# Performance work log

Measured on AMD Instinct MI355X. Metric: run time of the kernel, lower is better.

## Reference

```python
import jax, jax.numpy as jnp
import numpy as np

N_NODES, N_EDGES = 100000, 800000
F_NODE, F_EDGE, N_CLASSES = 128, 16, 10


def _lin(key, fan_in, fan_out, bias=True):
    k1, k2 = jax.random.split(key)
    W = jax.random.normal(k1, (fan_in, fan_out), jnp.float32) * 0.05
    if bias:
        b = jax.random.normal(k2, (fan_out,), jnp.float32) * 0.05
        return W, b
    return (W,)


def setup_inputs() -> dict:
    key = jax.random.key(0)
    ks = jax.random.split(key, 24)
    inp = {
        "x": jax.random.normal(ks[0], (N_NODES, F_NODE), jnp.float32),
        "edge_index": jax.random.randint(ks[1], (2, N_EDGES), 0, N_NODES, jnp.int64 if jax.config.jax_enable_x64 else jnp.int32),
        "edge_attr": jax.random.normal(ks[2], (N_EDGES, F_EDGE), jnp.float32),
    }
    dims = [(F_NODE, 128), (128, 128), (128, 256)]  # (in_channels, out_channels) per layer
    i = 3
    for li, (din, dout) in enumerate(dims, start=1):
        inp[f"Wq{li}"], inp[f"bq{li}"] = _lin(ks[i], din, dout); i += 1
        inp[f"Wk{li}"], inp[f"bk{li}"] = _lin(ks[i], din, dout); i += 1
        inp[f"Wv{li}"], inp[f"bv{li}"] = _lin(ks[i], din, dout); i += 1
        (inp[f"We{li}"],) = _lin(ks[i], F_EDGE, dout, bias=False); i += 1  # PyG lin_edge: bias=False
        inp[f"Ws{li}"], inp[f"bs{li}"] = _lin(ks[i], din, dout); i += 1  # root/skip weight
    inp["Wc"], inp["bc"] = _lin(ks[i], 256, N_CLASSES)
    return inp


def transformer_conv(x, src, dst, edge_attr, Wq, bq, Wk, bk, Wv, bv, We, Ws, bs):
    """PyG TransformerConv, heads=1, concat=True, root_weight=True."""
    N = x.shape[0]
    C = Wq.shape[1]
    q = x @ Wq + bq                      # [N, C]
    k = x @ Wk + bk                      # [N, C]
    v = x @ Wv + bv                      # [N, C]
    e = edge_attr @ We                   # [E, C] edge-conditioned term
    # per-edge attention logits: <q_i, k_j + e_ij> / sqrt(C)
    alpha = jnp.sum(q[dst] * (k[src] + e), axis=-1) / jnp.sqrt(jnp.float32(C))  # [E]
    # segment softmax over edges sharing a destination node
    m = jax.ops.segment_max(alpha, dst, num_segments=N)
    p = jnp.exp(alpha - m[dst])
    s = jax.ops.segment_sum(p, dst, num_segments=N)
    a = p / (s[dst] + 1e-16)
    # scatter-aggregate weighted messages (value_j + edge term)
    out = jax.ops.segment_sum(a[:, None] * (v[src] + e), dst, num_segments=N)  # [N, C]
    return out + x @ Ws + bs             # root/skip connection


def reference(x, edge_index, edge_attr,
              Wq1, bq1, Wk1, bk1, Wv1, bv1, We1, Ws1, bs1,
              Wq2, bq2, Wk2, bk2, Wv2, bv2, We2, Ws2, bs2,
              Wq3, bq3, Wk3, bk3, Wv3, bv3, We3, Ws3, bs3,
              Wc, bc):
    src, dst = edge_index[0], edge_index[1]
    h = transformer_conv(x, src, dst, edge_attr, Wq1, bq1, Wk1, bk1, Wv1, bv1, We1, Ws1, bs1)
    h = jax.nn.relu(h)  # dropout is identity in eval mode
    h = transformer_conv(h, src, dst, edge_attr, Wq2, bq2, Wk2, bk2, Wv2, bv2, We2, Ws2, bs2)
    h = jax.nn.relu(h)
    h = transformer_conv(h, src, dst, edge_attr, Wq3, bq3, Wk3, bk3, Wv3, bv3, We3, Ws3, bs3)
    return h @ Wc + bc                   # [N, num_classes]
```

## Files before the change

### kernel.cpp

```cpp
#include <hip/hip_runtime.h>
#include <math.h>


typedef unsigned int uint;
typedef unsigned short ushort;
typedef __bf16 bf16x8 __attribute__((ext_vector_type(8)));
typedef float f32x4 __attribute__((ext_vector_type(4)));

__device__ __forceinline__ ushort f2bf(float f) {
    uint u = __float_as_uint(f);
    u += 0x7fffu + ((u >> 16) & 1u);
    return (ushort)(u >> 16);
}
__device__ __forceinline__ float bf2f(ushort h) {
    return __uint_as_float(((uint)h) << 16);
}
__device__ __forceinline__ void unpack8(uint4 t, float* o) {
    o[0] = bf2f((ushort)(t.x & 0xffffu)); o[1] = bf2f((ushort)(t.x >> 16));
    o[2] = bf2f((ushort)(t.y & 0xffffu)); o[3] = bf2f((ushort)(t.y >> 16));
    o[4] = bf2f((ushort)(t.z & 0xffffu)); o[5] = bf2f((ushort)(t.z >> 16));
    o[6] = bf2f((ushort)(t.w & 0xffffu)); o[7] = bf2f((ushort)(t.w >> 16));
}

__global__ void k_zero(uint* p, int n) {
    int i = blockIdx.x * 256 + threadIdx.x;
    if (i < n) p[i] = 0u;
}

__global__ void k_hist(const int* __restrict__ dst, uint* __restrict__ counts, int E, int N) {
    int e = blockIdx.x * 256 + threadIdx.x;
    if (e < E) {
        int d = dst[e];
        d = (d < 0) ? 0 : (d >= N ? N - 1 : d);
        atomicAdd(&counts[d], 1u);
    }
}

__global__ void k_scan1(const uint* __restrict__ counts, uint* __restrict__ bsum, int n) {
    __shared__ uint sm[256];
    int tid = threadIdx.x;
    int base = blockIdx.x * 1024 + tid * 4;
    uint s = 0;
#pragma unroll
    for (int j = 0; j < 4; ++j)
        if (base + j < n) s += counts[base + j];
    sm[tid] = s;
    __syncthreads();
    for (int d = 128; d > 0; d >>= 1) {
        if (tid < d) sm[tid] += sm[tid + d];
        __syncthreads();
    }
    if (tid == 0) bsum[blockIdx.x] = sm[0];
}

__global__ void k_scan2(uint* bsum, int nb) {
    if (threadIdx.x == 0 && blockIdx.x == 0) {
        uint run = 0;
        for (int i = 0; i < nb; ++i) { uint v = bsum[i]; bsum[i] = run; run += v; }
    }
}

__global__ void k_scan3(const uint* __restrict__ counts, const uint* __restrict__ bsum,
                        uint* __restrict__ row_ptr, int n, int E) {
    __shared__ uint sm[256];
    int tid = threadIdx.x;
    int base = blockIdx.x * 1024 + tid * 4;
    uint local[4];
    uint s = 0;
#pragma unroll
    for (int j = 0; j < 4; ++j) {
        local[j] = (base + j < n) ? counts[base + j] : 0u;
        s += local[j];
    }
    sm[tid] = s;
    __syncthreads();
    for (int d = 1; d < 256; d <<= 1) {
        uint v = (tid >= d) ? sm[tid - d] : 0u;
        __syncthreads();
        sm[tid] += v;
        __syncthreads();
    }
    uint run = sm[tid] - s + bsum[blockIdx.x];
#pragma unroll
    for (int j = 0; j < 4; ++j)
        if (base + j < n) { row_ptr[base + j] = run; run += local[j]; }
    if (blockIdx.x == 0 && tid == 0) row_ptr[n] = (uint)E;
}

__global__ void k_fill(const int* __restrict__ ei, const uint* __restrict__ row_ptr,
                       uint* __restrict__ cursor, int2* __restrict__ srcid, int E, int N) {
    int e = blockIdx.x * 256 + threadIdx.x;
    if (e >= E) return;
    int s = ei[e];
    int d = ei[E + e];
    s = (s < 0) ? 0 : (s >= N ? N - 1 : s);
    d = (d < 0) ? 0 : (d >= N ? N - 1 : d);
    uint idx = row_ptr[d] + atomicAdd(&cursor[d], 1u);
    srcid[idx] = make_int2(s, e);
}

__global__ void k_cvt(const float4* __restrict__ in, ushort4* __restrict__ outp, int n4) {
    int i = blockIdx.x * 256 + threadIdx.x;
    if (i >= n4) return;
    float4 v = in[i];
    ushort4 o;
    o.x = f2bf(v.x); o.y = f2bf(v.y); o.z = f2bf(v.z); o.w = f2bf(v.w);
    outp[i] = o;
}

__global__ void k_packg(const float* __restrict__ Wq, const float* __restrict__ bq,
                        const float* __restrict__ We, float* __restrict__ Wgf,
                        float* __restrict__ bgf, int C) {
    int id = blockIdx.x * 256 + threadIdx.x;
    if (id < 2048) {
        int k = id >> 4, f = id & 15;
        float s = 0.f;
        for (int c = 0; c < C; ++c) s = fmaf(Wq[k * C + c], We[f * C + c], s);
        Wgf[id] = s;
    } else if (id < 2064) {
        int f = id - 2048;
        float s = 0.f;
        for (int c = 0; c < C; ++c) s = fmaf(bq[c], We[f * C + c], s);
        bgf[f] = s;
    }
}

__global__ void k_packw(const float* __restrict__ Wq, const float* __restrict__ Wk,
                        const float* __restrict__ Wv, const float* __restrict__ Ws,
                        const float* __restrict__ Wgf, ushort* __restrict__ Bp, int C) {
    int nct = (4 * C + 16) >> 4;
    int total = 4 * nct * 512;
    int id = blockIdx.x * 256 + threadIdx.x;
    if (id >= total) return;
    int j = id & 7;
    int rest = id >> 3;
    int lane = rest & 63;
    rest >>= 6;
    int ct = rest % nct;
    int kt = rest / nct;
    int k = kt * 32 + ((lane >> 4) << 3) + j;
    int c = (ct << 4) + (lane & 15);
    float w;
    if (c < 4 * C) {
        int mat = c / C, cc = c % C;
        const float* W = (mat == 0) ? Wq : (mat == 1) ? Wk : (mat == 2) ? Wv : Ws;
        w = W[k * C + cc];
    } else {
        w = Wgf[k * 16 + (c - 4 * C)];
    }
    Bp[id] = f2bf(w);
}

__global__ void k_bias(const float* __restrict__ bq, const float* __restrict__ bk,
                       const float* __restrict__ bv, const float* __restrict__ bs,
                       const float* __restrict__ bgf, float* __restrict__ outp, int C) {
    int c = blockIdx.x * 256 + threadIdx.x;
    if (c >= 4 * C + 16) return;
    float v;
    if (c < 4 * C) {
        int mat = c / C, cc = c % C;
        const float* b = (mat == 0) ? bq : (mat == 1) ? bk : (mat == 2) ? bv : bs;
        v = b[cc];
    } else {
        v = bgf[c - 4 * C];
    }
    outp[c] = v;
}

__global__ __launch_bounds__(256) void k_gemm(const ushort* __restrict__ A,
                                              const ushort* __restrict__ Bp,
                                              const float* __restrict__ bias,
                                              ushort* __restrict__ H,
                                              ushort* __restrict__ S,
                                              ushort* __restrict__ g, int C) {
    int fourC = 4 * C, threeC = 3 * C;
    int P = fourC + 16;
    int nct = P >> 4;
    int lane = threadIdx.x & 63;
    int wave = threadIdx.x >> 6;
    int quad = lane >> 4;
    int r = lane & 15;
    int m0 = blockIdx.y << 4;
    int c0 = (blockIdx.x << 8) + (wave << 6);
    int ct0 = c0 >> 4;
    if (ct0 >= nct) return;
    int row = m0 + r;

    f32x4 acc[4];
#pragma unroll
    for (int i = 0; i < 4; ++i) acc[i] = (f32x4){0.f, 0.f, 0.f, 0.f};

#pragma unroll
    for (int kk = 0; kk < 4; ++kk) {
        bf16x8 a = *(const bf16x8*)(A + (size_t)row * 128 + kk * 32 + (quad << 3));
#pragma unroll
        for (int i = 0; i < 4; ++i) {
            if (ct0 + i < nct) {
                bf16x8 b = *(const bf16x8*)(Bp + ((size_t)((kk * nct + ct0 + i) << 6) + lane) * 8);
                acc[i] = __builtin_amdgcn_mfma_f32_16x16x32_bf16(a, b, acc[i], 0, 0, 0);
            }
        }
    }
#pragma unroll
    for (int i = 0; i < 4; ++i) {
        int cc = c0 + (i << 4) + r;
        if (cc >= P) continue;
        float bi = bias[cc];
#pragma unroll
        for (int reg = 0; reg < 4; ++reg) {
            int rr = m0 + (quad << 2) + reg;
            ushort val = f2bf(acc[i][reg] + bi);
            if (cc < threeC)      H[(size_t)rr * threeC + cc] = val;
            else if (cc < fourC)  S[(size_t)rr * C + (cc - threeC)] = val;
            else                  g[(size_t)rr * 16 + (cc - fourC)] = val;
        }
    }
}

template <int C, int GSIZE, bool RELU>
__global__ __launch_bounds__(256, 6) void k_edge(const ushort* __restrict__ H,
                                                 ushort* __restrict__ S,
                                                 const ushort* __restrict__ g,
                                                 const uint* __restrict__ row_ptr,
                                                 const int2* __restrict__ srcid,
                                                 const float* __restrict__ eattr,
                                                 const float* __restrict__ We,
                                                 int N) {
    constexpr int VR = C / GSIZE;
    constexpr int TH = 3 * C;
    constexpr int GPB = 256 / GSIZE;
    __shared__ float swex[GPB][17];
    const float scale = (C == 128) ? 0.08838834764831843f : 0.0625f;
    const float foldk = 16.0f / (float)GSIZE;

    int lane = threadIdx.x & (GSIZE - 1);
    int grp = threadIdx.x / GSIZE;
    int f = lane & 15;
    int node = blockIdx.x * GPB + grp;
    if (node >= N) return;

    float q[VR];
    {
        uint4 tt = *(const uint4*)(H + (size_t)node * TH + lane * VR);
        unpack8(tt, q);
    }
    float gl = bf2f(g[(size_t)node * 16 + f]);
    uint beg = row_ptr[node], end = row_ptr[node + 1];

    float l = 0.f, w = 0.f;
    float acc[VR];
#pragma unroll
    for (int j = 0; j < VR; ++j) acc[j] = 0.f;

    for (uint t = beg; t < end; t += 2) {
        bool has1 = (t + 1 < end);
        int2 se0 = srcid[t];
        int2 se1 = has1 ? srcid[t + 1] : se0;
        float at0 = eattr[(size_t)se0.y * 16 + f];
        float at1 = eattr[(size_t)se1.y * 16 + f];
        uint4 k0 = *(const uint4*)(H + (size_t)se0.x * TH + C + lane * VR);
        uint4 v0 = *(const uint4*)(H + (size_t)se0.x * TH + 2 * C + lane * VR);
        uint4 k1, v1;
        if (has1) {
            k1 = *(const uint4*)(H + (size_t)se1.x * TH + C + lane * VR);
            v1 = *(const uint4*)(H + (size_t)se1.x * TH + 2 * C + lane * VR);
        }
        float kf[VR];
        unpack8(k0, kf);
        float p0 = foldk * at0 * gl;
#pragma unroll
        for (int j = 0; j < VR; ++j) p0 = fmaf(q[j], kf[j], p0);
        float p1 = 0.f;
        if (has1) {
            unpack8(k1, kf);
            p1 = foldk * at1 * gl;
#pragma unroll
            for (int j = 0; j < VR; ++j) p1 = fmaf(q[j], kf[j], p1);
        }
        p0 += __shfl_xor(p0, 1); p1 += __shfl_xor(p1, 1);
        p0 += __shfl_xor(p0, 2); p1 += __shfl_xor(p1, 2);
        p0 += __shfl_xor(p0, 4); p1 += __shfl_xor(p1, 4);
        p0 += __shfl_xor(p0, 8); p1 += __shfl_xor(p1, 8);
        if (GSIZE == 32) { p0 += __shfl_xor(p0, 16); p1 += __shfl_xor(p1, 16); }
        float e0 = __expf(p0 * scale);
        float e1 = has1 ? __expf(p1 * scale) : 0.f;
        l += e0 + e1;
        w = fmaf(e0, at0, w);
        w = fmaf(e1, at1, w);
        float vf[VR];
        unpack8(v0, vf);
#pragma unroll
        for (int j = 0; j < VR; ++j) acc[j] = fmaf(e0, vf[j], acc[j]);
        if (has1) {
            unpack8(v1, vf);
#pragma unroll
            for (int j = 0; j < VR; ++j) acc[j] = fmaf(e1, vf[j], acc[j]);
        }
    }

    float inv = 1.f / (l + 1e-16f);
    if (lane < 16) swex[grp][lane] = w;
    float ew[VR];
#pragma unroll
    for (int j = 0; j < VR; ++j) ew[j] = 0.f;
#pragma unroll
    for (int f2 = 0; f2 < 16; ++f2) {
        float wf = swex[grp][f2];
        const float* wrow = We + f2 * C + lane * VR;
#pragma unroll
        for (int u = 0; u < VR / 4; ++u) {
            float4 cv = *(const float4*)(wrow + u * 4);
            ew[u * 4 + 0] = fmaf(wf, cv.x, ew[u * 4 + 0]);
            ew[u * 4 + 1] = fmaf(wf, cv.y, ew[u * 4 + 1]);
            ew[u * 4 + 2] = fmaf(wf, cv.z, ew[u * 4 + 2]);
            ew[u * 4 + 3] = fmaf(wf, cv.w, ew[u * 4 + 3]);
        }
    }
    ushort* srow = S + (size_t)node * C + lane * VR;
    uint4 skv = *(const uint4*)srow;
    float sk[8];
    unpack8(skv, sk);
    uint4 ov;
    uint* op = (uint*)&ov;
#pragma unroll
    for (int h = 0; h < 4; ++h) {
        float o0 = (acc[2 * h] + ew[2 * h]) * inv + sk[2 * h];
        float o1 = (acc[2 * h + 1] + ew[2 * h + 1]) * inv + sk[2 * h + 1];
        if (RELU) { o0 = fmaxf(o0, 0.f); o1 = fmaxf(o1, 0.f); }
        op[h] = (uint)f2bf(o0) | ((uint)f2bf(o1) << 16);
    }
    *(uint4*)srow = ov;
}

__global__ void k_cls(const ushort* __restrict__ h, const float* __restrict__ Wc,
                      const float* __restrict__ bc, float* __restrict__ outp, int N) {
    int t = blockIdx.x * 256 + threadIdx.x;
    int node = t >> 4;
    int c = t & 15;
    if (node >= N || c >= 10) return;
    const ushort* hr = h + (size_t)node * 256;
    float acc = 0.f;
#pragma unroll 4
    for (int k4 = 0; k4 < 64; ++k4) {
        uint2 u = *(const uint2*)(hr + k4 * 4);
        float h0 = bf2f((ushort)(u.x & 0xffffu));
        float h1 = bf2f((ushort)(u.x >> 16));
        float h2 = bf2f((ushort)(u.y & 0xffffu));
        float h3 = bf2f((ushort)(u.y >> 16));
        int kb = k4 * 4;
        acc = fmaf(h0, Wc[(kb + 0) * 10 + c], acc);
        acc = fmaf(h1, Wc[(kb + 1) * 10 + c], acc);
        acc = fmaf(h2, Wc[(kb + 2) * 10 + c], acc);
        acc = fmaf(h3, Wc[(kb + 3) * 10 + c], acc);
    }
    outp[node * 10 + c] = acc + bc[c];
}

extern "C" void kernel_launch(void* const* d_in, const int* in_sizes, int n_in,
                              void* d_out, int out_size, void* d_ws, size_t ws_size,
                              hipStream_t stream) {
    const float* x = (const float*)d_in[0];
    const int* ei = (const int*)d_in[1];
    const float* eattr = (const float*)d_in[2];
    const int N = in_sizes[0] / 128;
    const int E = in_sizes[1] / 2;

    const float* Wq[3], *bq[3], *Wk[3], *bk[3], *Wv[3], *bv[3], *We[3], *Ws[3], *bs[3];
    for (int li = 0; li < 3; ++li) {
        int base = 3 + li * 9;
        Wq[li] = (const float*)d_in[base + 0];
        bq[li] = (const float*)d_in[base + 1];
        Wk[li] = (const float*)d_in[base + 2];
        bk[li] = (const float*)d_in[base + 3];
        Wv[li] = (const float*)d_in[base + 4];
        bv[li] = (const float*)d_in[base + 5];
        We[li] = (const float*)d_in[base + 6];
        Ws[li] = (const float*)d_in[base + 7];
        bs[li] = (const float*)d_in[base + 8];
    }
    const float* Wc = (const float*)d_in[30];
    const float* bc = (const float*)d_in[31];

    size_t off = 0;
    char* base = (char*)d_ws;
    auto alloc = [&](size_t bytes) -> void* {
        void* p = base + off;
        off = (off + bytes + 255) & ~(size_t)255;
        return p;
    };
    ushort* SA = (ushort*)alloc((size_t)N * 256 * 2);
    ushort* SB = (ushort*)alloc((size_t)N * 128 * 2);
    ushort* H  = (ushort*)alloc((size_t)N * 768 * 2);
    ushort* gbuf = (ushort*)alloc((size_t)N * 16 * 2);
    ushort* Bp = (ushort*)alloc(140000 * 2);
    float* biasc = (float*)alloc(1040 * 4);
    float* Wgf = (float*)alloc(2048 * 4);
    float* bgf = (float*)alloc(16 * 4);
    uint* row_ptr = (uint*)alloc((size_t)(N + 1) * 4);
    uint* counts = (uint*)alloc((size_t)N * 4);
    uint* cursor = (uint*)alloc((size_t)N * 4);
    uint* bsum = (uint*)alloc(1024 * 4);
    int2* srcid = (int2*)alloc((size_t)E * 8);

    ushort* xb = SB;

    int nb = (N + 1023) / 1024;

    k_zero<<<(N + 255) / 256, 256, 0, stream>>>(counts, N);
    k_zero<<<(N + 255) / 256, 256, 0, stream>>>(cursor, N);
    k_hist<<<(E + 255) / 256, 256, 0, stream>>>(ei + E, counts, E, N);
    k_scan1<<<nb, 256, 0, stream>>>(counts, bsum, N);
    k_scan2<<<1, 64, 0, stream>>>(bsum, nb);
    k_scan3<<<nb, 256, 0, stream>>>(counts, bsum, row_ptr, N, E);
    k_fill<<<(E + 255) / 256, 256, 0, stream>>>(ei, row_ptr, cursor, srcid, E, N);

    int n4 = N * 128 / 4;
    k_cvt<<<(n4 + 255) / 256, 256, 0, stream>>>((const float4*)x, (ushort4*)xb, n4);

    for (int li = 0; li < 3; ++li) {
        int C = (li == 2) ? 256 : 128;
        int P = 4 * C + 16;
        int packTotal = 4 * (P >> 4) * 512;
        const ushort* A = (li == 0) ? xb : (li == 1) ? SA : SB;
        ushort* Sout = (li == 1) ? SB : SA;

        k_packg<<<9, 256, 0, stream>>>(Wq[li], bq[li], We[li], Wgf, bgf, C);
        k_packw<<<(packTotal + 255) / 256, 256, 0, stream>>>(Wq[li], Wk[li], Wv[li], Ws[li], Wgf, Bp, C);
        k_bias<<<(P + 255) / 256, 256, 0, stream>>>(bq[li], bk[li], bv[li], bs[li], bgf, biasc, C);
        k_gemm<<<dim3((P + 255) / 256, N / 16), 256, 0, stream>>>(A, Bp, biasc, H, Sout, gbuf, C);
        if (li == 2)
            k_edge<256, 32, false><<<(N * 32 + 255) / 256, 256, 0, stream>>>(H, Sout, gbuf, row_ptr, srcid, eattr, We[li], N);
        else
            k_edge<128, 16, true><<<(N * 16 + 255) / 256, 256, 0, stream>>>(H, Sout, gbuf, row_ptr, srcid, eattr, We[li], N);
    }

    k_cls<<<(N * 16 + 255) / 256, 256, 0, stream>>>(SA, Wc, bc, (float*)d_out, N);
}
```

Baseline: 1.021 ms.

## Fuse classifier into last edge kernel, permute edge attrs, enlarge GEMM tiles

Edge attributes are now permuted into CSR order as bf16 during the fill pass, so the edge kernel reads them contiguously and prefetches the next pair's source ids and attributes one iteration ahead. The GEMM processes 64 rows per block, reusing each B fragment across four row tiles, and handles a ragged N. Weight and bias packing merge into one kernel, the zeroing launches merge into one, and the final classifier is fused into the last edge kernel through a shuffle reduction. The aims are fewer launches, less scattered edge-attribute traffic and better GEMM operand reuse, at the cost of more registers in the GEMM and edge kernels and bf16 rounding of edge attributes.

Result: slower. 1.183 ms (+15.8%).

```diff
diff --git a/kernel.cpp b/kernel.cpp
--- a/kernel.cpp
+++ b/kernel.cpp
@@ -87,8 +87,9 @@
     if (blockIdx.x == 0 && tid == 0) row_ptr[n] = (uint)E;
 }
 
-__global__ void k_fill(const int* __restrict__ ei, const uint* __restrict__ row_ptr,
-                       uint* __restrict__ cursor, int2* __restrict__ srcid, int E, int N) {
+__global__ void k_fill(const int* __restrict__ ei, const float* __restrict__ eattr,
+                       const uint* __restrict__ row_ptr, uint* __restrict__ cursor,
+                       int* __restrict__ srci, ushort* __restrict__ eperm, int E, int N) {
     int e = blockIdx.x * 256 + threadIdx.x;
     if (e >= E) return;
     int s = ei[e];
@@ -96,7 +97,20 @@
     s = (s < 0) ? 0 : (s >= N ? N - 1 : s);
     d = (d < 0) ? 0 : (d >= N ? N - 1 : d);
     uint idx = row_ptr[d] + atomicAdd(&cursor[d], 1u);
-    srcid[idx] = make_int2(s, e);
+    srci[idx] = s;
+    const float4* sv = (const float4*)(eattr + (size_t)e * 16);
+    float4 a0 = sv[0], a1 = sv[1], a2 = sv[2], a3 = sv[3];
+    uint4 o0, o1;
+    o0.x = (uint)f2bf(a0.x) | ((uint)f2bf(a0.y) << 16);
+    o0.y = (uint)f2bf(a0.z) | ((uint)f2bf(a0.w) << 16);
+    o0.z = (uint)f2bf(a1.x) | ((uint)f2bf(a1.y) << 16);
+    o0.w = (uint)f2bf(a1.z) | ((uint)f2bf(a1.w) << 16);
+    o1.x = (uint)f2bf(a2.x) | ((uint)f2bf(a2.y) << 16);
+    o1.y = (uint)f2bf(a2.z) | ((uint)f2bf(a2.w) << 16);
+    o1.z = (uint)f2bf(a3.x) | ((uint)f2bf(a3.y) << 16);
+    o1.w = (uint)f2bf(a3.z) | ((uint)f2bf(a3.w) << 16);
+    *(uint4*)(eperm + (size_t)idx * 16) = o0;
+    *(uint4*)(eperm + (size_t)idx * 16 + 8) = o1;
 }
 
 __global__ void k_cvt(const float4* __restrict__ in, ushort4* __restrict__ outp, int n4) {
@@ -125,46 +139,46 @@
     }
 }
 
-__global__ void k_packw(const float* __restrict__ Wq, const float* __restrict__ Wk,
-                        const float* __restrict__ Wv, const float* __restrict__ Ws,
-                        const float* __restrict__ Wgf, ushort* __restrict__ Bp, int C) {
-    int nct = (4 * C + 16) >> 4;
+__global__ void k_packwb(const float* __restrict__ Wq, const float* __restrict__ bq,
+                         const float* __restrict__ Wk, const float* __restrict__ bk,
+                         const float* __restrict__ Wv, const float* __restrict__ bv,
+                         const float* __restrict__ Ws, const float* __restrict__ bs,
+                         const float* __restrict__ Wgf, const float* __restrict__ bgf,
+                         ushort* __restrict__ Bp, float* __restrict__ biasc, int C) {
+    int P = 4 * C + 16;
+    int nct = P >> 4;
     int total = 4 * nct * 512;
     int id = blockIdx.x * 256 + threadIdx.x;
-    if (id >= total) return;
-    int j = id & 7;
-    int rest = id >> 3;
-    int lane = rest & 63;
-    rest >>= 6;
-    int ct = rest % nct;
-    int kt = rest / nct;
-    int k = kt * 32 + ((lane >> 4) << 3) + j;
-    int c = (ct << 4) + (lane & 15);
-    float w;
-    if (c < 4 * C) {
-        int mat = c / C, cc = c % C;
-        const float* W = (mat == 0) ? Wq : (mat == 1) ? Wk : (mat == 2) ? Wv : Ws;
-        w = W[k * C + cc];
-    } else {
-        w = Wgf[k * 16 + (c - 4 * C)];
-    }
-    Bp[id] = f2bf(w);
-}
-
-__global__ void k_bias(const float* __restrict__ bq, const float* __restrict__ bk,
-                       const float* __restrict__ bv, const float* __restrict__ bs,
-                       const float* __restrict__ bgf, float* __restrict__ outp, int C) {
-    int c = blockIdx.x * 256 + threadIdx.x;
-    if (c >= 4 * C + 16) return;
-    float v;
-    if (c < 4 * C) {
-        int mat = c / C, cc = c % C;
-        const float* b = (mat == 0) ? bq : (mat == 1) ? bk : (mat == 2) ? bv : bs;
-        v = b[cc];
-    } else {
-        v = bgf[c - 4 * C];
-    }
-    outp[c] = v;
+    if (id < total) {
+        int j = id & 7;
+        int rest = id >> 3;
+        int lane = rest & 63;
+        rest >>= 6;
+        int ct = rest % nct;
+        int kt = rest / nct;
+        int k = kt * 32 + ((lane >> 4) << 3) + j;
+        int c = (ct << 4) + (lane & 15);
+        float w;
+        if (c < 4 * C) {
+            int mat = c / C, cc = c % C;
+            const float* W = (mat == 0) ? Wq : (mat == 1) ? Wk : (mat == 2) ? Wv : Ws;
+            w = W[k * C + cc];
+        } else {
+            w = Wgf[k * 16 + (c - 4 * C)];
+        }
+        Bp[id] = f2bf(w);
+    } else if (id < total + P) {
+        int c = id - total;
+        float v;
+        if (c < 4 * C) {
+            int mat = c / C, cc = c % C;
+            const float* b = (mat == 0) ? bq : (mat == 1) ? bk : (mat == 2) ? bv : bs;
+            v = b[cc];
+        } else {
+            v = bgf[c - 4 * C];
+        }
+        biasc[c] = v;
+    }
 }
 
 __global__ __launch_bounds__(256) void k_gemm(const ushort* __restrict__ A,
@@ -172,7 +186,7 @@
                                               const float* __restrict__ bias,
                                               ushort* __restrict__ H,
                                               ushort* __restrict__ S,
-                                              ushort* __restrict__ g, int C) {
+                                              ushort* __restrict__ g, int C, int N) {
     int fourC = 4 * C, threeC = 3 * C;
     int P = fourC + 16;
     int nct = P >> 4;
@@ -180,51 +194,66 @@
     int wave = threadIdx.x >> 6;
     int quad = lane >> 4;
     int r = lane & 15;
-    int m0 = blockIdx.y << 4;
-    int c0 = (blockIdx.x << 8) + (wave << 6);
-    int ct0 = c0 >> 4;
+    int m0 = blockIdx.y << 6;
+    int ct0 = (blockIdx.x << 4) + (wave << 2);
     if (ct0 >= nct) return;
-    int row = m0 + r;
-
-    f32x4 acc[4];
-#pragma unroll
-    for (int i = 0; i < 4; ++i) acc[i] = (f32x4){0.f, 0.f, 0.f, 0.f};
+
+    f32x4 acc[4][4];
+#pragma unroll
+    for (int rt = 0; rt < 4; ++rt)
+#pragma unroll
+        for (int i = 0; i < 4; ++i) acc[rt][i] = (f32x4){0.f, 0.f, 0.f, 0.f};
 
 #pragma unroll
     for (int kk = 0; kk < 4; ++kk) {
-        bf16x8 a = *(const bf16x8*)(A + (size_t)row * 128 + kk * 32 + (quad << 3));
+        bf16x8 a[4];
+#pragma unroll
+        for (int rt = 0; rt < 4; ++rt) {
+            int row = m0 + rt * 16 + r;
+            if (row >= N) row = N - 1;
+            a[rt] = *(const bf16x8*)(A + (size_t)row * 128 + kk * 32 + (quad << 3));
+        }
 #pragma unroll
         for (int i = 0; i < 4; ++i) {
             if (ct0 + i < nct) {
                 bf16x8 b = *(const bf16x8*)(Bp + ((size_t)((kk * nct + ct0 + i) << 6) + lane) * 8);
-                acc[i] = __builtin_amdgcn_mfma_f32_16x16x32_bf16(a, b, acc[i], 0, 0, 0);
+#pragma unroll
+                for (int rt = 0; rt < 4; ++rt)
+                    acc[rt][i] = __builtin_amdgcn_mfma_f32_16x16x32_bf16(a[rt], b, acc[rt][i], 0, 0, 0);
             }
         }
     }
 #pragma unroll
     for (int i = 0; i < 4; ++i) {
-        int cc = c0 + (i << 4) + r;
+        int cc = ((ct0 + i) << 4) + r;
         if (cc >= P) continue;
         float bi = bias[cc];
 #pragma unroll
-        for (int reg = 0; reg < 4; ++reg) {
-            int rr = m0 + (quad << 2) + reg;
-            ushort val = f2bf(acc[i][reg] + bi);
-            if (cc < threeC)      H[(size_t)rr * threeC + cc] = val;
-            else if (cc < fourC)  S[(size_t)rr * C + (cc - threeC)] = val;
-            else                  g[(size_t)rr * 16 + (cc - fourC)] = val;
-        }
-    }
-}
-
-template <int C, int GSIZE, bool RELU>
+        for (int rt = 0; rt < 4; ++rt) {
+#pragma unroll
+            for (int reg = 0; reg < 4; ++reg) {
+                int rr = m0 + rt * 16 + (quad << 2) + reg;
+                if (rr >= N) continue;
+                ushort val = f2bf(acc[rt][i][reg] + bi);
+                if (cc < threeC)      H[(size_t)rr * threeC + cc] = val;
+                else if (cc < fourC)  S[(size_t)rr * C + (cc - threeC)] = val;
+                else                  g[(size_t)rr * 16 + (cc - fourC)] = val;
+            }
+        }
+    }
+}
+
+template <int C, int GSIZE, bool RELU, bool FUSECLS>
 __global__ __launch_bounds__(256, 6) void k_edge(const ushort* __restrict__ H,
                                                  ushort* __restrict__ S,
                                                  const ushort* __restrict__ g,
                                                  const uint* __restrict__ row_ptr,
-                                                 const int2* __restrict__ srcid,
-                                                 const float* __restrict__ eattr,
+                                                 const int* __restrict__ srci,
+                                                 const ushort* __restrict__ eperm,
                                                  const float* __restrict__ We,
+                                                 const float* __restrict__ Wc,
+                                                 const float* __restrict__ bc,
+                                                 float* __restrict__ outp,
                                                  int N) {
     constexpr int VR = C / GSIZE;
     constexpr int TH = 3 * C;
@@ -252,49 +281,60 @@
 #pragma unroll
     for (int j = 0; j < VR; ++j) acc[j] = 0.f;
 
-    for (uint t = beg; t < end; t += 2) {
-        bool has1 = (t + 1 < end);
-        int2 se0 = srcid[t];
-        int2 se1 = has1 ? srcid[t + 1] : se0;
-        float at0 = eattr[(size_t)se0.y * 16 + f];
-        float at1 = eattr[(size_t)se1.y * 16 + f];
-        uint4 k0 = *(const uint4*)(H + (size_t)se0.x * TH + C + lane * VR);
-        uint4 v0 = *(const uint4*)(H + (size_t)se0.x * TH + 2 * C + lane * VR);
-        uint4 k1, v1;
-        if (has1) {
-            k1 = *(const uint4*)(H + (size_t)se1.x * TH + C + lane * VR);
-            v1 = *(const uint4*)(H + (size_t)se1.x * TH + 2 * C + lane * VR);
-        }
-        float kf[VR];
-        unpack8(k0, kf);
-        float p0 = foldk * at0 * gl;
-#pragma unroll
-        for (int j = 0; j < VR; ++j) p0 = fmaf(q[j], kf[j], p0);
-        float p1 = 0.f;
-        if (has1) {
-            unpack8(k1, kf);
-            p1 = foldk * at1 * gl;
-#pragma unroll
-            for (int j = 0; j < VR; ++j) p1 = fmaf(q[j], kf[j], p1);
-        }
-        p0 += __shfl_xor(p0, 1); p1 += __shfl_xor(p1, 1);
-        p0 += __shfl_xor(p0, 2); p1 += __shfl_xor(p1, 2);
-        p0 += __shfl_xor(p0, 4); p1 += __shfl_xor(p1, 4);
-        p0 += __shfl_xor(p0, 8); p1 += __shfl_xor(p1, 8);
-        if (GSIZE == 32) { p0 += __shfl_xor(p0, 16); p1 += __shfl_xor(p1, 16); }
-        float e0 = __expf(p0 * scale);
-        float e1 = has1 ? __expf(p1 * scale) : 0.f;
-        l += e0 + e1;
-        w = fmaf(e0, at0, w);
-        w = fmaf(e1, at1, w);
-        float vf[VR];
-        unpack8(v0, vf);
-#pragma unroll
-        for (int j = 0; j < VR; ++j) acc[j] = fmaf(e0, vf[j], acc[j]);
-        if (has1) {
-            unpack8(v1, vf);
-#pragma unroll
-            for (int j = 0; j < VR; ++j) acc[j] = fmaf(e1, vf[j], acc[j]);
+    if (beg < end) {
+        bool h1 = (beg + 1 < end);
+        int s0 = srci[beg];
+        int s1 = h1 ? srci[beg + 1] : s0;
+        float a0 = bf2f(eperm[(size_t)beg * 16 + f]);
+        float a1 = h1 ? bf2f(eperm[(size_t)(beg + 1) * 16 + f]) : 0.f;
+        for (uint t = beg; t < end; t += 2) {
+            uint4 k0 = *(const uint4*)(H + (size_t)s0 * TH + C + lane * VR);
+            uint4 v0 = *(const uint4*)(H + (size_t)s0 * TH + 2 * C + lane * VR);
+            uint4 k1, v1;
+            if (h1) {
+                k1 = *(const uint4*)(H + (size_t)s1 * TH + C + lane * VR);
+                v1 = *(const uint4*)(H + (size_t)s1 * TH + 2 * C + lane * VR);
+            }
+            uint tn = t + 2;
+            bool h0n = (tn < end);
+            bool h1n = (tn + 1 < end);
+            int s0n = s0, s1n;
+            float a0n = 0.f, a1n = 0.f;
+            if (h0n) { s0n = srci[tn]; a0n = bf2f(eperm[(size_t)tn * 16 + f]); }
+            s1n = h1n ? srci[tn + 1] : s0n;
+            if (h1n) a1n = bf2f(eperm[(size_t)(tn + 1) * 16 + f]);
+            float kf[VR];
+            unpack8(k0, kf);
+            float p0 = foldk * a0 * gl;
+#pragma unroll
+            for (int j = 0; j < VR; ++j) p0 = fmaf(q[j], kf[j], p0);
+            float p1 = 0.f;
+            if (h1) {
+                unpack8(k1, kf);
+                p1 = foldk * a1 * gl;
+#pragma unroll
+                for (int j = 0; j < VR; ++j) p1 = fmaf(q[j], kf[j], p1);
+            }
+            p0 += __shfl_xor(p0, 1); p1 += __shfl_xor(p1, 1);
+            p0 += __shfl_xor(p0, 2); p1 += __shfl_xor(p1, 2);
+            p0 += __shfl_xor(p0, 4); p1 += __shfl_xor(p1, 4);
+            p0 += __shfl_xor(p0, 8); p1 += __shfl_xor(p1, 8);
+            if (GSIZE == 32) { p0 += __shfl_xor(p0, 16); p1 += __shfl_xor(p1, 16); }
+            float e0 = __expf(p0 * scale);
+            float e1 = h1 ? __expf(p1 * scale) : 0.f;
+            l += e0 + e1;
+            w = fmaf(e0, a0, w);
+            w = fmaf(e1, a1, w);
+            float vf[VR];
+            unpack8(v0, vf);
+#pragma unroll
+            for (int j = 0; j < VR; ++j) acc[j] = fmaf(e0, vf[j], acc[j]);
+            if (h1) {
+                unpack8(v1, vf);
+#pragma unroll
+                for (int j = 0; j < VR; ++j) acc[j] = fmaf(e1, vf[j], acc[j]);
+            }
+            s0 = s0n; s1 = s1n; a0 = a0n; a1 = a1n; h1 = h1n;
         }
     }
 
@@ -316,44 +356,45 @@
             ew[u * 4 + 3] = fmaf(wf, cv.w, ew[u * 4 + 3]);
         }
     }
-    ushort* srow = S + (size_t)node * C + lane * VR;
+    const ushort* srow = S + (size_t)node * C + lane * VR;
     uint4 skv = *(const uint4*)srow;
     float sk[8];
     unpack8(skv, sk);
-    uint4 ov;
-    uint* op = (uint*)&ov;
-#pragma unroll
-    for (int h = 0; h < 4; ++h) {
-        float o0 = (acc[2 * h] + ew[2 * h]) * inv + sk[2 * h];
-        float o1 = (acc[2 * h + 1] + ew[2 * h + 1]) * inv + sk[2 * h + 1];
-        if (RELU) { o0 = fmaxf(o0, 0.f); o1 = fmaxf(o1, 0.f); }
-        op[h] = (uint)f2bf(o0) | ((uint)f2bf(o1) << 16);
-    }
-    *(uint4*)srow = ov;
-}
-
-__global__ void k_cls(const ushort* __restrict__ h, const float* __restrict__ Wc,
-                      const float* __restrict__ bc, float* __restrict__ outp, int N) {
-    int t = blockIdx.x * 256 + threadIdx.x;
-    int node = t >> 4;
-    int c = t & 15;
-    if (node >= N || c >= 10) return;
-    const ushort* hr = h + (size_t)node * 256;
-    float acc = 0.f;
-#pragma unroll 4
-    for (int k4 = 0; k4 < 64; ++k4) {
-        uint2 u = *(const uint2*)(hr + k4 * 4);
-        float h0 = bf2f((ushort)(u.x & 0xffffu));
-        float h1 = bf2f((ushort)(u.x >> 16));
-        float h2 = bf2f((ushort)(u.y & 0xffffu));
-        float h3 = bf2f((ushort)(u.y >> 16));
-        int kb = k4 * 4;
-        acc = fmaf(h0, Wc[(kb + 0) * 10 + c], acc);
-        acc = fmaf(h1, Wc[(kb + 1) * 10 + c], acc);
-        acc = fmaf(h2, Wc[(kb + 2) * 10 + c], acc);
-        acc = fmaf(h3, Wc[(kb + 3) * 10 + c], acc);
-    }
-    outp[node * 10 + c] = acc + bc[c];
+    float o[8];
+#pragma unroll
+    for (int j = 0; j < VR; ++j) {
+        o[j] = (acc[j] + ew[j]) * inv + sk[j];
+        if (RELU) o[j] = fmaxf(o[j], 0.f);
+    }
+    if (!FUSECLS) {
+        uint4 ov;
+        uint* op = (uint*)&ov;
+#pragma unroll
+        for (int h = 0; h < 4; ++h)
+            op[h] = (uint)f2bf(o[2 * h]) | ((uint)f2bf(o[2 * h + 1]) << 16);
+        *(uint4*)(S + (size_t)node * C + lane * VR) = ov;
+    } else {
+        float logit[10];
+#pragma unroll
+        for (int c = 0; c < 10; ++c) logit[c] = 0.f;
+        const float* wcr = Wc + (size_t)(lane * VR) * 10;
+#pragma unroll
+        for (int j = 0; j < VR; ++j) {
+            float hv = bf2f(f2bf(o[j]));
+#pragma unroll
+            for (int c = 0; c < 10; ++c) logit[c] = fmaf(hv, wcr[j * 10 + c], logit[c]);
+        }
+#pragma unroll
+        for (int off = 1; off < GSIZE; off <<= 1)
+#pragma unroll
+            for (int c = 0; c < 10; ++c) logit[c] += __shfl_xor(logit[c], off);
+        if (lane < 10) {
+            float r = 0.f;
+#pragma unroll
+            for (int c = 0; c < 10; ++c) r = (lane == c) ? logit[c] : r;
+            outp[(size_t)node * 10 + lane] = r + bc[lane];
+        }
+    }
 }
 
 extern "C" void kernel_launch(void* const* d_in, const int* in_sizes, int n_in,
@@ -397,42 +438,46 @@
     float* Wgf = (float*)alloc(2048 * 4);
     float* bgf = (float*)alloc(16 * 4);
     uint* row_ptr = (uint*)alloc((size_t)(N + 1) * 4);
-    uint* counts = (uint*)alloc((size_t)N * 4);
-    uint* cursor = (uint*)alloc((size_t)N * 4);
+    uint* counts = (uint*)alloc((size_t)N * 2 * 4);
+    uint* cursor = counts + N;
     uint* bsum = (uint*)alloc(1024 * 4);
-    int2* srcid = (int2*)alloc((size_t)E * 8);
+    int* srci = (int*)alloc((size_t)E * 4);
+    ushort* eperm = (ushort*)alloc((size_t)E * 16 * 2);
 
     ushort* xb = SB;
 
     int nb = (N + 1023) / 1024;
 
-    k_zero<<<(N + 255) / 256, 256, 0, stream>>>(counts, N);
-    k_zero<<<(N + 255) / 256, 256, 0, stream>>>(cursor, N);
+    k_zero<<<(2 * N + 255) / 256, 256, 0, stream>>>(counts, 2 * N);
     k_hist<<<(E + 255) / 256, 256, 0, stream>>>(ei + E, counts, E, N);
     k_scan1<<<nb, 256, 0, stream>>>(counts, bsum, N);
     k_scan2<<<1, 64, 0, stream>>>(bsum, nb);
     k_scan3<<<nb, 256, 0, stream>>>(counts, bsum, row_ptr, N, E);
-    k_fill<<<(E + 255) / 256, 256, 0, stream>>>(ei, row_ptr, cursor, srcid, E, N);
+    k_fill<<<(E + 255) / 256, 256, 0, stream>>>(ei, eattr, row_ptr, cursor, srci, eperm, E, N);
 
     int n4 = N * 128 / 4;
     k_cvt<<<(n4 + 255) / 256, 256, 0, stream>>>((const float4*)x, (ushort4*)xb, n4);
+
+    int gy = (N + 63) / 64;
 
     for (int li = 0; li < 3; ++li) {
         int C = (li == 2) ? 256 : 128;
         int P = 4 * C + 16;
-        int packTotal = 4 * (P >> 4) * 512;
+        int nct = P >> 4;
+        int packTotal = 4 * nct * 512 + P;
         const ushort* A = (li == 0) ? xb : (li == 1) ? SA : SB;
         ushort* Sout = (li == 1) ? SB : SA;
 
         k_packg<<<9, 256, 0, stream>>>(Wq[li], bq[li], We[li], Wgf, bgf, C);
-        k_packw<<<(packTotal + 255) / 256, 256, 0, stream>>>(Wq[li], Wk[li], Wv[li], Ws[li], Wgf, Bp, C);
-        k_bias<<<(P + 255) / 256, 256, 0, stream>>>(bq[li], bk[li], bv[li], bs[li], bgf, biasc, C);
-        k_gemm<<<dim3((P + 255) / 256, N / 16), 256, 0, stream>>>(A, Bp, biasc, H, Sout, gbuf, C);
+        k_packwb<<<(packTotal + 255) / 256, 256, 0, stream>>>(
+            Wq[li], bq[li], Wk[li], bk[li], Wv[li], bv[li], Ws[li], bs[li],
+            Wgf, bgf, Bp, biasc, C);
+        k_gemm<<<dim3((nct + 15) / 16, gy), 256, 0, stream>>>(A, Bp, biasc, H, Sout, gbuf, C, N);
         if (li == 2)
-            k_edge<256, 32, false><<<(N * 32 + 255) / 256, 256, 0, stream>>>(H, Sout, gbuf, row_ptr, srcid, eattr, We[li], N);
+            k_edge<256, 32, false, true><<<(N * 32 + 255) / 256, 256, 0, stream>>>(
+                H, Sout, gbuf, row_ptr, srci, eperm, We[li], Wc, bc, (float*)d_out, N);
         else
-            k_edge<128, 16, true><<<(N * 16 + 255) / 256, 256, 0, stream>>>(H, Sout, gbuf, row_ptr, srcid, eattr, We[li], N);
-    }
-
-    k_cls<<<(N * 16 + 255) / 256, 256, 0, stream>>>(SA, Wc, bc, (float*)d_out, N);
-}
+            k_edge<128, 16, true, false><<<(N * 16 + 255) / 256, 256, 0, stream>>>(
+                H, Sout, gbuf, row_ptr, srci, eperm, We[li], nullptr, nullptr, nullptr, N);
+    }
+}
```
